# Optimization experiments

Measured on AMD Instinct MI355X. Metric: run time of the kernel, lower is better.

## Reference

```python
import jax, jax.numpy as jnp
import numpy as np
from jax import lax

EPS = 1e-8

def int8_fq(x):
    # Int8ActPerTensorFloat: per-tensor float scale from runtime max-abs, fake-quant with STE.
    s = jnp.maximum(jnp.max(jnp.abs(x)) / 127.0, EPS)
    q = jnp.clip(jnp.round(x / s), -128.0, 127.0) * s
    return x + lax.stop_gradient(q - x)

def bin_w(w):
    # BINARY weight quant: per-tensor scale = mean(|w|), weights -> +/- scale (STE).
    s = jnp.mean(jnp.abs(w))
    wq = jnp.where(w >= 0, s, -s)
    return w + lax.stop_gradient(wq - w)

def qrelu(x):
    # QuantReLU with int8 input_quant and int8 act_quant
    return int8_fq(jax.nn.relu(int8_fq(x)))

def conv2d(x, w, b):
    y = lax.conv_general_dilated(x, w, window_strides=(1, 1), padding='VALID',
                                 dimension_numbers=('NCHW', 'OIHW', 'NCHW'))
    return y + b[None, :, None, None]

def maxpool2(x):
    return lax.reduce_window(x, -jnp.inf, lax.max, (1, 1, 2, 2), (1, 1, 2, 2), 'VALID')

def setup_inputs() -> dict:
    key = jax.random.key(0)
    ks = jax.random.split(key, 12)
    B = 16384
    inp = {
        'input_tensor': jax.random.normal(ks[0], (B, 3, 32, 32), dtype=jnp.float32),
        'w1': jax.random.normal(ks[1], (6, 3, 5, 5), dtype=jnp.float32) * 0.1,
        'b1': jax.random.normal(ks[2], (6,), dtype=jnp.float32) * 0.01,
        'w2': jax.random.normal(ks[3], (16, 6, 5, 5), dtype=jnp.float32) * 0.1,
        'b2': jax.random.normal(ks[4], (16,), dtype=jnp.float32) * 0.01,
        'fw1': jax.random.normal(ks[5], (120, 400), dtype=jnp.float32) * 0.05,
        'fb1': jax.random.normal(ks[6], (120,), dtype=jnp.float32) * 0.01,
        'fw2': jax.random.normal(ks[7], (84, 120), dtype=jnp.float32) * 0.05,
        'fb2': jax.random.normal(ks[8], (84,), dtype=jnp.float32) * 0.01,
        'fw3': jax.random.normal(ks[9], (10, 84), dtype=jnp.float32) * 0.05,
        'fb3': jax.random.normal(ks[10], (10,), dtype=jnp.float32) * 0.01,
    }
    return inp

def reference(input_tensor, w1, b1, w2, b2, fw1, fb1, fw2, fb2, fw3, fb3):
    x = int8_fq(input_tensor)                  # QuantIdentity
    x = qrelu(conv2d(x, bin_w(w1), b1))        # conv1 + relu1: [B,6,28,28]
    x = maxpool2(x)                            # [B,6,14,14]
    x = qrelu(conv2d(x, bin_w(w2), b2))        # conv2 + relu2: [B,16,10,10]
    x = maxpool2(x)                            # [B,16,5,5]
    x = x.reshape(x.shape[0], -1)              # [B,400]
    x = qrelu(x @ bin_w(fw1).T + fb1)          # fc1 + relu3: [B,120]
    x = qrelu(x @ bin_w(fw2).T + fb2)          # fc2 + relu4: [B,84]
    out = x @ bin_w(fw3).T + fb3               # fc3: [B,10]
    return out
```

## Files before the change

### kernel.cpp

```cpp
#include <hip/hip_runtime.h>
#include <math.h>

#define BATCH 16384
#define EPSQ 1e-8f

#define OFF_SCAL 0
#define OFF_WPK1 16
#define OFF_WPK2 196
#define OFF_FQ1  1156
#define OFF_FQ2  13156
#define OFF_FQ3  15844
#define OFF_A    16384
#define OFF_QIN   OFF_A
#define OFF_QC2   OFF_A
#define OFF_ISUM2 (OFF_A + 6400000)
#define OFF_QC3   (OFF_A + 10000000)
#define OFF_P3    (OFF_A + 12000000)
#define OFF_P4    (OFF_A + 14000000)
#define OFF_ISUM1 (OFF_A + 18874368)

__device__ inline int sdot4(unsigned int a, unsigned int b, int c) {
    return __builtin_amdgcn_sdot4((int)a, (int)b, c, false);
}

__device__ inline unsigned int fkey(float f) {
    unsigned int u = __float_as_uint(f);
    return (u & 0x80000000u) ? ~u : (u | 0x80000000u);
}
__device__ inline float fdec(unsigned int k) {
    unsigned int u = (k & 0x80000000u) ? (k ^ 0x80000000u) : ~k;
    return __uint_as_float(u);
}
#define KEY_ZERO   0x80000000u
#define KEY_NEGINF 0x007FFFFFu

__device__ inline float waveMax(float v) {
    #pragma unroll
    for (int off = 32; off > 0; off >>= 1)
        v = fmaxf(v, __shfl_down(v, off, 64));
    return v;
}

__device__ inline void blockAtomicMax2(float vmax, float vnmax,
                                       unsigned int* gmax, unsigned int* gnmax) {
    __shared__ float sm[4], sn[4];
    float a = waveMax(vmax), b = waveMax(vnmax);
    int tid = threadIdx.x;
    if ((tid & 63) == 0) { sm[tid >> 6] = a; sn[tid >> 6] = b; }
    __syncthreads();
    if (tid == 0) {
        atomicMax(gmax, fkey(fmaxf(fmaxf(sm[0], sm[1]), fmaxf(sm[2], sm[3]))));
        atomicMax(gnmax, fkey(fmaxf(fmaxf(sn[0], sn[1]), fmaxf(sn[2], sn[3]))));
    }
}

__device__ inline float fq_elem(float x, float s) {
    float q = fminf(fmaxf(rintf(x / s), -128.0f), 127.0f);
    return q * s;
}
__device__ inline int qrelu_code(float x, float s1, float s2) {
    float q = fq_elem(x, s1);
    q = fmaxf(q, 0.0f);
    return (int)fminf(fmaxf(rintf(q / s2), -128.0f), 127.0f);
}
__device__ inline void get_qrelu_scales(const unsigned int* scalu, int slot,
                                        float& s1, float& s2) {
    float maxa = fdec(scalu[slot]), negm = fdec(scalu[slot + 1]);
    float absm = fmaxf(maxa, negm);
    s1 = fmaxf(absm / 127.0f, EPSQ);
    float qm = fminf(fmaxf(rintf(maxa / s1), -128.0f), 127.0f) * s1;
    s2 = fmaxf(fmaxf(qm, 0.0f) / 127.0f, EPSQ);
}

__device__ inline unsigned int sgn8(float w) { return (w >= 0.0f) ? 0x01u : 0xFFu; }

__device__ inline unsigned int u32at(const unsigned int* wv, int wi, int k) {
    return (k == 0) ? wv[wi]
        : __builtin_amdgcn_perm(wv[wi + 1], wv[wi], 0x03020100u + 0x01010101u * (unsigned)k);
}

__global__ __launch_bounds__(256) void prep_kernel(const float* __restrict__ w1,
        const float* __restrict__ w2, const float* __restrict__ fw1,
        const float* __restrict__ fw2, const float* __restrict__ fw3,
        float* __restrict__ wsf) {
    int blk = blockIdx.x, tid = threadIdx.x;
    unsigned int* wsu = (unsigned int*)wsf;
    if (blk == 0) {
        if (tid == 0) wsu[0] = KEY_ZERO;
        else if (tid <= 8) wsu[tid] = KEY_NEGINF;
        return;
    }
    const float* src = nullptr; int N = 0;
    if (blk == 1)      { src = w1;  N = 450; }
    else if (blk == 2) { src = w2;  N = 2400; }
    else if (blk == 3) { src = fw1; N = 48000; }
    else if (blk == 4) { src = fw2; N = 10080; }
    else               { src = fw3; N = 840; }
    __shared__ float red[256];
    float partial = 0.0f;
    for (int i = tid; i < N; i += 256) partial += fabsf(src[i]);
    red[tid] = partial;
    __syncthreads();
    for (int s = 128; s > 0; s >>= 1) {
        if (tid < s) red[tid] += red[tid + s];
        __syncthreads();
    }
    if (tid == 0) wsf[8 + blk] = red[0] / (float)N;

    if (blk == 1) {
        for (int t = tid; t < 90; t += 256) {
            const float* wp = w1 + t * 5;
            wsu[OFF_WPK1 + 2*t] = sgn8(wp[0]) | (sgn8(wp[1])<<8) | (sgn8(wp[2])<<16) | (sgn8(wp[3])<<24);
            wsu[OFF_WPK1 + 2*t + 1] = sgn8(wp[4]) << 24;
        }
    } else if (blk == 2) {
        for (int t = tid; t < 480; t += 256) {
            const float* wp = w2 + t * 5;
            wsu[OFF_WPK2 + 2*t] = sgn8(wp[0]) | (sgn8(wp[1])<<8) | (sgn8(wp[2])<<16) | (sgn8(wp[3])<<24);
            wsu[OFF_WPK2 + 2*t + 1] = sgn8(wp[4]) << 24;
        }
    } else if (blk == 3) {
        for (int i = tid; i < 12000; i += 256) {
            int j = i / 100, k = i % 100;
            const float* wp = fw1 + j * 400 + k * 4;
            wsu[OFF_FQ1 + i] = sgn8(wp[0]) | (sgn8(wp[1])<<8) | (sgn8(wp[2])<<16) | (sgn8(wp[3])<<24);
        }
    } else if (blk == 4) {
        for (int i = tid; i < 2688; i += 256) {
            int j = i >> 5, k = i & 31;
            unsigned int u = 0;
            if (k < 30) {
                const float* wp = fw2 + j * 120 + k * 4;
                u = sgn8(wp[0]) | (sgn8(wp[1])<<8) | (sgn8(wp[2])<<16) | (sgn8(wp[3])<<24);
            }
            wsu[OFF_FQ2 + i] = u;
        }
    } else {
        for (int i = tid; i < 240; i += 256) {
            int j = i / 24, k = i % 24;
            unsigned int u = 0;
            if (k < 21) {
                const float* wp = fw3 + j * 84 + k * 4;
                u = sgn8(wp[0]) | (sgn8(wp[1])<<8) | (sgn8(wp[2])<<16) | (sgn8(wp[3])<<24);
            }
            wsu[OFF_FQ3 + i] = u;
        }
    }
}

__global__ __launch_bounds__(256) void absmax_kernel(const float4* __restrict__ x, int n4,
                                                     unsigned int* __restrict__ gkey) {
    float m = 0.0f;
    int stride = gridDim.x * 256;
    for (int i = blockIdx.x * 256 + threadIdx.x; i < n4; i += stride) {
        float4 v = x[i];
        m = fmaxf(m, fmaxf(fmaxf(fabsf(v.x), fabsf(v.y)), fmaxf(fabsf(v.z), fabsf(v.w))));
    }
    __shared__ float sm[4];
    m = waveMax(m);
    int tid = threadIdx.x;
    if ((tid & 63) == 0) sm[tid >> 6] = m;
    __syncthreads();
    if (tid == 0)
        atomicMax(gkey, fkey(fmaxf(fmaxf(sm[0], sm[1]), fmaxf(sm[2], sm[3]))));
}

__global__ __launch_bounds__(256) void quant1_kernel(const float4* __restrict__ x,
                                                     float* __restrict__ wsf) {
    unsigned int* wsu = (unsigned int*)wsf;
    float s0 = fmaxf(fdec(wsu[0]) / 127.0f, EPSQ);
    unsigned int* qin = wsu + OFF_QIN;
    int stride = gridDim.x * 256;
    const int total = BATCH * 96 * 12;
    for (int unit = blockIdx.x * 256 + threadIdx.x; unit < total; unit += stride) {
        int row_id = unit / 12, w = unit % 12;
        int plane = row_id >> 5, row = row_id & 31;
        int slot = (row >> 1) + ((row & 1) << 4);
        unsigned int u = 0;
        if (w < 8) {
            float4 v = x[row_id * 8 + w];
            int q0 = (int)fminf(fmaxf(rintf(v.x / s0), -128.f), 127.f);
            int q1 = (int)fminf(fmaxf(rintf(v.y / s0), -128.f), 127.f);
            int q2 = (int)fminf(fmaxf(rintf(v.z / s0), -128.f), 127.f);
            int q3 = (int)fminf(fmaxf(rintf(v.w / s0), -128.f), 127.f);
            u = (q0 & 255) | ((q1 & 255) << 8) | ((q2 & 255) << 16) | ((unsigned)(q3 & 255) << 24);
        }
        qin[(plane * 32 + slot) * 12 + w] = u;
    }
}

#define C1_ROWP 48
#define C1_CIS  1536
#define C1_IMGS 4608
#define C1_NIMG 8

template<int PH>
__device__ __forceinline__ void c1_phase(const unsigned char* ib, const unsigned int* wcp,
                                         int* ip, int& gmax, int& gmin) {
    int a0[14], a1[14];
    #pragma unroll
    for (int i = 0; i < 14; i++) { a0[i] = 0; a1[i] = 0; }
    #pragma unroll 1
    for (int ci = 0; ci < 3; ci++) {
        uint4 A[6]; unsigned int Bv[6];
        const unsigned char* cb = ib + ci * C1_CIS;
        #pragma unroll
        for (int r = 0; r < 6; r++) {
            const unsigned char* rb = cb + (((r & 1) << 4) + (r >> 1)) * C1_ROWP;
            if (PH == 0) {
                A[r]  = *(const uint4*)(rb);
                Bv[r] = *(const unsigned int*)(rb + 16);
            } else {
                Bv[r] = *(const unsigned int*)(rb + 12);
                A[r]  = *(const uint4*)(rb + 16);
            }
        }
        const unsigned int* wkp = wcp + ci * 10;
        unsigned int wk0[5], wk4[5];
        #pragma unroll
        for (int ky = 0; ky < 5; ky++) { wk0[ky] = wkp[2*ky]; wk4[ky] = wkp[2*ky+1]; }
        #pragma unroll
        for (int r6 = 0; r6 < 6; r6++) {
            unsigned int wv[5];
            if (PH == 0) {
                wv[0] = A[r6].x; wv[1] = A[r6].y; wv[2] = A[r6].z; wv[3] = A[r6].w; wv[4] = Bv[r6];
            } else {
                wv[0] = Bv[r6]; wv[1] = A[r6].x; wv[2] = A[r6].y; wv[3] = A[r6].z; wv[4] = A[r6].w;
            }
            const int OFS = (PH == 0) ? 0 : 2;
            unsigned int up[15];
            #pragma unroll
            for (int i = 0; i < 15; i++) {
                int e = OFS + i;
                up[i] = u32at(wv, e >> 2, e & 3);
            }
            if (r6 <= 4) {
                unsigned int w0 = wk0[r6], w4 = wk4[r6];
                #pragma unroll
                for (int i = 0; i < 14; i++) {
                    a0[i] = sdot4(up[i], w0, a0[i]);
                    a0[i] = sdot4(up[i+1], w4, a0[i]);
                }
            }
            if (r6 >= 1) {
                unsigned int w0 = wk0[r6-1], w4 = wk4[r6-1];
                #pragma unroll
                for (int i = 0; i < 14; i++) {
                    a1[i] = sdot4(up[i], w0, a1[i]);
                    a1[i] = sdot4(up[i+1], w4, a1[i]);
                }
            }
        }
    }
    #pragma unroll
    for (int i = 0; i < 14; i++) {
        gmax = max(gmax, max(a0[i], a1[i]));
        gmin = min(gmin, min(a0[i], a1[i]));
    }
    #pragma unroll
    for (int p = 0; p < 7; p++)
        ip[p] = max(max(a0[2*p], a0[2*p+1]), max(a1[2*p], a1[2*p+1]));
}

__global__ __launch_bounds__(256) void conv1_kernel(const float* __restrict__ b1,
                                                    float* __restrict__ wsf) {
    __shared__ __align__(16) unsigned char xq[C1_NIMG * C1_IMGS];
    __shared__ unsigned int wpk[180];
    __shared__ float bsm[6];
    unsigned int* wsu = (unsigned int*)wsf;
    int tid = threadIdx.x;
    int b0 = blockIdx.x * C1_NIMG;
    float s0 = fmaxf(fdec(wsu[0]) / 127.0f, EPSQ);
    float seff = s0 * wsf[9];

    {
        const uint4* src = (const uint4*)((const unsigned char*)(wsu + OFF_QIN) + (size_t)b0 * C1_IMGS);
        uint4* dst = (uint4*)xq;
        for (int i = tid; i < C1_NIMG * 288; i += 256) dst[i] = src[i];
    }
    for (int i = tid; i < 180; i += 256) wpk[i] = wsu[OFF_WPK1 + i];
    if (tid < 6) bsm[tid] = b1[tid];
    __syncthreads();

    unsigned int* isum1 = wsu + OFF_ISUM1;
    float vmax = -INFINITY, vnmax = -INFINITY;
    const int ntask = C1_NIMG * 84;
    for (int t = tid; t < ntask; t += 256) {
        int img = t / 84, r = t % 84;
        int c = r / 14, py = r % 14;
        const unsigned char* ib = &xq[img * C1_IMGS + py * C1_ROWP];
        const unsigned int* wcp = &wpk[c * 30];
        int ip0[7], ip1[7];
        int gmax = -2000000000, gmin = 2000000000;
        c1_phase<0>(ib, wcp, ip0, gmax, gmin);
        c1_phase<1>(ib, wcp, ip1, gmax, gmin);
        float bias = bsm[c];
        vmax  = fmaxf(vmax,  fmaf(seff, (float)gmax, bias));
        vnmax = fmaxf(vnmax, -fmaf(seff, (float)gmin, bias));
        unsigned int* dst = isum1 + 588 * (size_t)(b0 + img) + 7 * (c * 14 + py);
        int v14[14];
        #pragma unroll
        for (int p = 0; p < 7; p++) { v14[p] = ip0[p]; v14[7 + p] = ip1[p]; }
        #pragma unroll
        for (int p = 0; p < 7; p++)
            dst[p] = (v14[2*p] & 0xFFFF) | ((unsigned)(v14[2*p+1] & 0xFFFF) << 16);
    }
    blockAtomicMax2(vmax, vnmax, wsu + 1, wsu + 2);
}

__global__ __launch_bounds__(256) void quant2_kernel(const float* __restrict__ b1,
                                                     float* __restrict__ wsf) {
    unsigned int* wsu = (unsigned int*)wsf;
    float s1, s2;
    get_qrelu_scales(wsu, 1, s1, s2);
    float s0 = fmaxf(fdec(wsu[0]) / 127.0f, EPSQ);
    float seff = s0 * wsf[9];
    float bv[6];
    #pragma unroll
    for (int c = 0; c < 6; c++) bv[c] = b1[c];
    const short* isum1 = (const short*)(wsu + OFF_ISUM1);
    unsigned int* qc2 = wsu + OFF_QC2;
    int stride = gridDim.x * 256;
    const int total = BATCH * 84 * 4;
    for (int unit = blockIdx.x * 256 + threadIdx.x; unit < total; unit += stride) {
        int row_id = unit >> 2, w = unit & 3;
        int bci = row_id / 14, row = row_id % 14;
        int ci = bci % 6;
        int slot = (row >> 1) + ((row & 1) << 3);
        float bias = bv[ci];
        unsigned int u = 0;
        const short* sp = isum1 + (size_t)bci * 196 + row * 14;
        #pragma unroll
        for (int k = 0; k < 4; k++) {
            int col = w * 4 + k;
            int code = 0;
            if (col < 14) {
                float pre = fmaf(seff, (float)sp[col], bias);
                code = qrelu_code(pre, s1, s2);
            }
            u |= ((unsigned)(code & 255)) << (8 * k);
        }
        qc2[((size_t)bci * 16 + slot) * 4 + w] = u;
    }
}

#define C2_ROWP 16
#define C2_CIS  256
#define C2_IMGS 1536
#define C2_NIMG 12

__global__ __launch_bounds__(256) void conv2_kernel(const float* __restrict__ b2,
                                                    float* __restrict__ wsf) {
    __shared__ __align__(16) unsigned char act[C2_NIMG * C2_IMGS];
    __shared__ unsigned int wpk[960];
    __shared__ float bsm[16];
    __shared__ __align__(16) short spb[C2_NIMG * 400];
    unsigned int* wsu = (unsigned int*)wsf;
    int tid = threadIdx.x;
    int b0 = blockIdx.x * C2_NIMG;
    int nimg = min(C2_NIMG, BATCH - b0);
    float s1, s2;
    get_qrelu_scales(wsu, 1, s1, s2);
    float seff = s2 * wsf[10];

    {
        const uint4* src = (const uint4*)((const unsigned char*)(wsu + OFF_QC2) + (size_t)b0 * C2_IMGS);
        uint4* dst = (uint4*)act;
        for (int i = tid; i < nimg * 96; i += 256) dst[i] = src[i];
    }
    for (int i = tid; i < 960; i += 256) wpk[i] = wsu[OFF_WPK2 + i];
    if (tid < 16) bsm[tid] = b2[tid];
    __syncthreads();

    float vmax = -INFINITY, vnmax = -INFINITY;
    int ntask = nimg * 20;
    if (tid < ntask) {
        int img = tid / 20, rem = tid % 20;
        int cq = rem / 5, py = rem % 5;
        int c0 = cq * 4;
        const unsigned char* ib = &act[img * C2_IMGS + py * C2_ROWP];
        int a0[4][10], a1[4][10];
        #pragma unroll
        for (int cc = 0; cc < 4; cc++)
            #pragma unroll
            for (int i = 0; i < 10; i++) { a0[cc][i] = 0; a1[cc][i] = 0; }
        #pragma unroll 1
        for (int ci = 0; ci < 6; ci++) {
            uint4 R[6];
            #pragma unroll
            for (int r6 = 0; r6 < 6; r6++)
                R[r6] = *(const uint4*)(ib + ci * C2_CIS + (((r6 & 1) << 3) + (r6 >> 1)) * C2_ROWP);
            #pragma unroll
            for (int r6 = 0; r6 < 6; r6++) {
                unsigned int wv[4] = { R[r6].x, R[r6].y, R[r6].z, R[r6].w };
                unsigned int up[11];
                #pragma unroll
                for (int i = 0; i < 11; i++) up[i] = u32at(wv, i >> 2, i & 3);
                #pragma unroll
                for (int cc = 0; cc < 4; cc++) {
                    const unsigned int* wkp = &wpk[((c0 + cc) * 6 + ci) * 10];
                    if (r6 <= 4) {
                        unsigned int w0 = wkp[2 * r6], w4 = wkp[2 * r6 + 1];
                        #pragma unroll
                        for (int i = 0; i < 10; i++) {
                            a0[cc][i] = sdot4(up[i], w0, a0[cc][i]);
                            a0[cc][i] = sdot4(up[i + 1], w4, a0[cc][i]);
                        }
                    }
                    if (r6 >= 1) {
                        unsigned int w0 = wkp[2 * (r6 - 1)], w4 = wkp[2 * (r6 - 1) + 1];
                        #pragma unroll
                        for (int i = 0; i < 10; i++) {
                            a1[cc][i] = sdot4(up[i], w0, a1[cc][i]);
                            a1[cc][i] = sdot4(up[i + 1], w4, a1[cc][i]);
                        }
                    }
                }
            }
        }
        #pragma unroll
        for (int cc = 0; cc < 4; cc++) {
            int gmax = -2000000000, gmin = 2000000000;
            #pragma unroll
            for (int i = 0; i < 10; i++) {
                gmax = max(gmax, max(a0[cc][i], a1[cc][i]));
                gmin = min(gmin, min(a0[cc][i], a1[cc][i]));
            }
            float bias = bsm[c0 + cc];
            vmax  = fmaxf(vmax,  fmaf(seff, (float)gmax, bias));
            vnmax = fmaxf(vnmax, -fmaf(seff, (float)gmin, bias));
            short* dst = spb + img * 400 + (c0 + cc) * 25 + py * 5;
            #pragma unroll
            for (int p = 0; p < 5; p++)
                dst[p] = (short)max(max(a0[cc][2*p], a0[cc][2*p+1]),
                                    max(a1[cc][2*p], a1[cc][2*p+1]));
        }
    }
    __syncthreads();
    {
        const uint4* pb4 = (const uint4*)spb;
        uint4* d4 = (uint4*)((short*)(wsu + OFF_ISUM2) + (size_t)b0 * 400);
        for (int i = tid; i < nimg * 50; i += 256) d4[i] = pb4[i];
    }
    blockAtomicMax2(vmax, vnmax, wsu + 3, wsu + 4);
}

__global__ __launch_bounds__(256) void quant3_kernel(const float* __restrict__ b2,
                                                     float* __restrict__ wsf) {
    unsigned int* wsu = (unsigned int*)wsf;
    float s1, s2;
    get_qrelu_scales(wsu, 3, s1, s2);
    float sp1, sp2;
    get_qrelu_scales(wsu, 1, sp1, sp2);
    float seff = sp2 * wsf[10];
    __shared__ float bv[16];
    if (threadIdx.x < 16) bv[threadIdx.x] = b2[threadIdx.x];
    __syncthreads();
    const short* isum2 = (const short*)(wsu + OFF_ISUM2);
    unsigned int* qc3 = wsu + OFF_QC3;
    int stride = gridDim.x * 256;
    const int total = BATCH * 100;
    for (int unit = blockIdx.x * 256 + threadIdx.x; unit < total; unit += stride) {
        int b = unit / 100, w = unit % 100;
        const short* sp = isum2 + (size_t)b * 400 + w * 4;
        unsigned int u = 0;
        #pragma unroll
        for (int k = 0; k < 4; k++) {
            int p = w * 4 + k;
            float pre = fmaf(seff, (float)sp[k], bv[p / 25]);
            int code = qrelu_code(pre, s1, s2);
            u |= ((unsigned)(code & 255)) << (8 * k);
        }
        qc3[unit] = u;
    }
}

__global__ __launch_bounds__(256) void fc1_kernel(const float* __restrict__ fb1,
                                                  float* __restrict__ wsf) {
    __shared__ unsigned int xs[32][100];
    __shared__ __align__(16) float pb[32 * 120];
    unsigned int* wsu = (unsigned int*)wsf;
    float* p3 = wsf + OFF_P3;
    int tid = threadIdx.x;
    size_t row0 = (size_t)blockIdx.x * 32;
    float s1, s2;
    get_qrelu_scales(wsu, 3, s1, s2);
    float seff = s2 * wsf[11];
    {
        const uint4* src = (const uint4*)(wsu + OFF_QC3 + row0 * 100);
        uint4* dst = (uint4*)xs;
        for (int i = tid; i < 800; i += 256) dst[i] = src[i];
    }
    __syncthreads();
    float vmax = -INFINITY, vnmax = -INFINITY;
    if (tid < 240) {
        int g = tid / 120, j = tid % 120;
        int acc[16];
        #pragma unroll
        for (int r = 0; r < 16; r++) acc[r] = 0;
        const uint4* wrow = (const uint4*)&wsu[OFF_FQ1 + j * 100];
        for (int kg = 0; kg < 25; kg++) {
            uint4 wv = wrow[kg];
            #pragma unroll
            for (int r = 0; r < 16; r++) {
                uint4 xv = *(const uint4*)&xs[g * 16 + r][kg * 4];
                acc[r] = sdot4(xv.x, wv.x, acc[r]);
                acc[r] = sdot4(xv.y, wv.y, acc[r]);
                acc[r] = sdot4(xv.z, wv.z, acc[r]);
                acc[r] = sdot4(xv.w, wv.w, acc[r]);
            }
        }
        float bias = fb1[j];
        #pragma unroll
        for (int r = 0; r < 16; r++) {
            float pv = fmaf(seff, (float)acc[r], bias);
            pb[(g * 16 + r) * 120 + j] = pv;
            vmax = fmaxf(vmax, pv); vnmax = fmaxf(vnmax, -pv);
        }
    }
    __syncthreads();
    {
        const float4* pb4 = (const float4*)pb;
        float4* d4 = (float4*)(p3 + row0 * 120);
        for (int i = tid; i < 960; i += 256) d4[i] = pb4[i];
    }
    blockAtomicMax2(vmax, vnmax, wsu + 5, wsu + 6);
}

__global__ __launch_bounds__(256) void fc2_kernel(const float* __restrict__ fb2,
                                                  float* __restrict__ wsf) {
    __shared__ unsigned int xs[48][32];
    __shared__ __align__(16) float pb[48 * 84];
    unsigned int* wsu = (unsigned int*)wsf;
    const float* p3 = wsf + OFF_P3;
    float* p4 = wsf + OFF_P4;
    int tid = threadIdx.x;
    size_t row0 = (size_t)blockIdx.x * 48;
    int nrow = min(48, (int)(BATCH - row0));
    float s1, s2;
    get_qrelu_scales(wsu, 5, s1, s2);
    float seff = s2 * wsf[12];
    const float4* src = (const float4*)(p3 + row0 * 120);
    for (int i = tid; i < nrow * 30; i += 256) {
        float4 v = src[i];
        int c0 = qrelu_code(v.x, s1, s2), c1 = qrelu_code(v.y, s1, s2);
        int c2 = qrelu_code(v.z, s1, s2), c3 = qrelu_code(v.w, s1, s2);
        xs[i / 30][i % 30] = c0 | (c1 << 8) | (c2 << 16) | ((unsigned)c3 << 24);
    }
    if (tid < 48) { xs[tid][30] = 0; xs[tid][31] = 0; }
    __syncthreads();
    float vmax = -INFINITY, vnmax = -INFINITY;
    if (tid < 252) {
        int g = tid / 84, j = tid % 84;
        int acc[16];
        #pragma unroll
        for (int r = 0; r < 16; r++) acc[r] = 0;
        const uint4* wrow = (const uint4*)&wsu[OFF_FQ2 + j * 32];
        #pragma unroll
        for (int kg = 0; kg < 8; kg++) {
            uint4 wv = wrow[kg];
            #pragma unroll
            for (int r = 0; r < 16; r++) {
                uint4 xv = *(const uint4*)&xs[g * 16 + r][kg * 4];
                acc[r] = sdot4(xv.x, wv.x, acc[r]);
                acc[r] = sdot4(xv.y, wv.y, acc[r]);
                acc[r] = sdot4(xv.z, wv.z, acc[r]);
                acc[r] = sdot4(xv.w, wv.w, acc[r]);
            }
        }
        float bias = fb2[j];
        #pragma unroll
        for (int r = 0; r < 16; r++) {
            int lr = g * 16 + r;
            if (lr < nrow) {
                float pv = fmaf(seff, (float)acc[r], bias);
                pb[lr * 84 + j] = pv;
                vmax = fmaxf(vmax, pv); vnmax = fmaxf(vnmax, -pv);
            }
        }
    }
    __syncthreads();
    {
        const float4* pb4 = (const float4*)pb;
        float4* d4 = (float4*)(p4 + row0 * 84);
        for (int i = tid; i < nrow * 21; i += 256) d4[i] = pb4[i];
    }
    blockAtomicMax2(vmax, vnmax, wsu + 7, wsu + 8);
}

__global__ __launch_bounds__(256) void fc3_kernel(const float* __restrict__ fb3,
                                                  float* __restrict__ out,
                                                  float* __restrict__ wsf) {
    __shared__ unsigned int wsm[240];
    __shared__ float bs[10];
    __shared__ __align__(16) float pb[2560];
    unsigned int* wsu = (unsigned int*)wsf;
    const float* p4 = wsf + OFF_P4;
    int tid = threadIdx.x;
    for (int i = tid; i < 240; i += 256) wsm[i] = wsu[OFF_FQ3 + i];
    if (tid < 10) bs[tid] = fb3[tid];
    __syncthreads();
    float s1, s2;
    get_qrelu_scales(wsu, 7, s1, s2);
    float seff = s2 * wsf[13];
    size_t row = (size_t)blockIdx.x * 256 + tid;
    unsigned int xr[24];
    const float4* src = (const float4*)(p4 + row * 84);
    #pragma unroll
    for (int k = 0; k < 21; k++) {
        float4 v = src[k];
        int c0 = qrelu_code(v.x, s1, s2), c1 = qrelu_code(v.y, s1, s2);
        int c2 = qrelu_code(v.z, s1, s2), c3 = qrelu_code(v.w, s1, s2);
        xr[k] = c0 | (c1 << 8) | (c2 << 16) | ((unsigned)c3 << 24);
    }
    xr[21] = 0; xr[22] = 0; xr[23] = 0;
    #pragma unroll
    for (int j = 0; j < 10; j++) {
        int acc = 0;
        #pragma unroll
        for (int k = 0; k < 24; k++) acc = sdot4(xr[k], wsm[j * 24 + k], acc);
        pb[tid * 10 + j] = fmaf(seff, (float)acc, bs[j]);
    }
    __syncthreads();
    {
        const float4* pb4 = (const float4*)pb;
        float4* d4 = (float4*)(out + (size_t)blockIdx.x * 2560);
        for (int i = tid; i < 640; i += 256) d4[i] = pb4[i];
    }
}

extern "C" void kernel_launch(void* const* d_in, const int* in_sizes, int n_in,
                              void* d_out, int out_size, void* d_ws, size_t ws_size,
                              hipStream_t stream) {
    const float* input = (const float*)d_in[0];
    const float* w1  = (const float*)d_in[1];
    const float* b1  = (const float*)d_in[2];
    const float* w2  = (const float*)d_in[3];
    const float* b2  = (const float*)d_in[4];
    const float* fw1 = (const float*)d_in[5];
    const float* fb1 = (const float*)d_in[6];
    const float* fw2 = (const float*)d_in[7];
    const float* fb2 = (const float*)d_in[8];
    const float* fw3 = (const float*)d_in[9];
    const float* fb3 = (const float*)d_in[10];
    float* ws  = (float*)d_ws;
    float* out = (float*)d_out;

    prep_kernel<<<6, 256, 0, stream>>>(w1, w2, fw1, fw2, fw3, ws);
    absmax_kernel<<<2048, 256, 0, stream>>>((const float4*)input,
                                            (int)((size_t)BATCH * 3072 / 4),
                                            (unsigned int*)ws);
    quant1_kernel<<<8192, 256, 0, stream>>>((const float4*)input, ws);
    conv1_kernel<<<BATCH / C1_NIMG, 256, 0, stream>>>(b1, ws);
    quant2_kernel<<<4096, 256, 0, stream>>>(b1, ws);
    conv2_kernel<<<(BATCH + C2_NIMG - 1) / C2_NIMG, 256, 0, stream>>>(b2, ws);
    quant3_kernel<<<2048, 256, 0, stream>>>(b2, ws);
    fc1_kernel<<<BATCH / 32, 256, 0, stream>>>(fb1, ws);
    fc2_kernel<<<(BATCH + 47) / 48, 256, 0, stream>>>(fb2, ws);
    fc3_kernel<<<BATCH / 256, 256, 0, stream>>>(fb3, out, ws);
}
```

Baseline: 470.0 us.

## Fuse qrelu requantization passes into conv2 and fc1 kernel prologues

Removes the standalone quant2 and quant3 kernels. conv2 now reads the pooled int16 conv1 sums and applies the qrelu quantization while filling its shared-memory tile, and fc1 does the same for the conv2 sums. This drops two kernel launches and the write-then-read round trip of the int8 code buffers through global memory. The cost is extra scalar ALU work and less coalesced short loads inside the consumer kernels' load phases. Act tiles in conv2 that were previously copied as zero padding are no longer written, so correctness depends on whether those padding bytes are read.

```diff
diff --git a/kernel.cpp b/kernel.cpp
--- a/kernel.cpp
+++ b/kernel.cpp
@@ -12,9 +12,7 @@
 #define OFF_FQ3  15844
 #define OFF_A    16384
 #define OFF_QIN   OFF_A
-#define OFF_QC2   OFF_A
 #define OFF_ISUM2 (OFF_A + 6400000)
-#define OFF_QC3   (OFF_A + 10000000)
 #define OFF_P3    (OFF_A + 12000000)
 #define OFF_P4    (OFF_A + 14000000)
 #define OFF_ISUM1 (OFF_A + 18874368)
@@ -308,52 +306,18 @@
     blockAtomicMax2(vmax, vnmax, wsu + 1, wsu + 2);
 }
 
-__global__ __launch_bounds__(256) void quant2_kernel(const float* __restrict__ b1,
-                                                     float* __restrict__ wsf) {
-    unsigned int* wsu = (unsigned int*)wsf;
-    float s1, s2;
-    get_qrelu_scales(wsu, 1, s1, s2);
-    float s0 = fmaxf(fdec(wsu[0]) / 127.0f, EPSQ);
-    float seff = s0 * wsf[9];
-    float bv[6];
-    #pragma unroll
-    for (int c = 0; c < 6; c++) bv[c] = b1[c];
-    const short* isum1 = (const short*)(wsu + OFF_ISUM1);
-    unsigned int* qc2 = wsu + OFF_QC2;
-    int stride = gridDim.x * 256;
-    const int total = BATCH * 84 * 4;
-    for (int unit = blockIdx.x * 256 + threadIdx.x; unit < total; unit += stride) {
-        int row_id = unit >> 2, w = unit & 3;
-        int bci = row_id / 14, row = row_id % 14;
-        int ci = bci % 6;
-        int slot = (row >> 1) + ((row & 1) << 3);
-        float bias = bv[ci];
-        unsigned int u = 0;
-        const short* sp = isum1 + (size_t)bci * 196 + row * 14;
-        #pragma unroll
-        for (int k = 0; k < 4; k++) {
-            int col = w * 4 + k;
-            int code = 0;
-            if (col < 14) {
-                float pre = fmaf(seff, (float)sp[col], bias);
-                code = qrelu_code(pre, s1, s2);
-            }
-            u |= ((unsigned)(code & 255)) << (8 * k);
-        }
-        qc2[((size_t)bci * 16 + slot) * 4 + w] = u;
-    }
-}
-
 #define C2_ROWP 16
 #define C2_CIS  256
 #define C2_IMGS 1536
 #define C2_NIMG 12
 
-__global__ __launch_bounds__(256) void conv2_kernel(const float* __restrict__ b2,
+__global__ __launch_bounds__(256) void conv2_kernel(const float* __restrict__ b1,
+                                                    const float* __restrict__ b2,
                                                     float* __restrict__ wsf) {
     __shared__ __align__(16) unsigned char act[C2_NIMG * C2_IMGS];
     __shared__ unsigned int wpk[960];
     __shared__ float bsm[16];
+    __shared__ float b1s[6];
     __shared__ __align__(16) short spb[C2_NIMG * 400];
     unsigned int* wsu = (unsigned int*)wsf;
     int tid = threadIdx.x;
@@ -361,15 +325,30 @@
     int nimg = min(C2_NIMG, BATCH - b0);
     float s1, s2;
     get_qrelu_scales(wsu, 1, s1, s2);
+    float s0 = fmaxf(fdec(wsu[0]) / 127.0f, EPSQ);
+    float seff1 = s0 * wsf[9];
     float seff = s2 * wsf[10];
+    if (tid < 6) b1s[tid] = b1[tid];
+    if (tid < 16) bsm[tid] = b2[tid];
+    for (int i = tid; i < 960; i += 256) wpk[i] = wsu[OFF_WPK2 + i];
+    __syncthreads();
 
     {
-        const uint4* src = (const uint4*)((const unsigned char*)(wsu + OFF_QC2) + (size_t)b0 * C2_IMGS);
-        uint4* dst = (uint4*)act;
-        for (int i = tid; i < nimg * 96; i += 256) dst[i] = src[i];
-    }
-    for (int i = tid; i < 960; i += 256) wpk[i] = wsu[OFF_WPK2 + i];
-    if (tid < 16) bsm[tid] = b2[tid];
+        const short* isum1 = (const short*)(wsu + OFF_ISUM1);
+        for (int i = tid; i < nimg * 588; i += 256) {
+            int img = i / 588, rem = i % 588;
+            int e = rem * 2;
+            int ci = e / 196, r2 = e % 196;
+            int row = r2 / 14, col = r2 % 14;
+            const short* sp = isum1 + (size_t)(b0 + img) * 1176 + e;
+            float bias = b1s[ci];
+            int r0 = qrelu_code(fmaf(seff1, (float)sp[0], bias), s1, s2);
+            int r1 = qrelu_code(fmaf(seff1, (float)sp[1], bias), s1, s2);
+            int slot = (row >> 1) + ((row & 1) << 3);
+            *(unsigned short*)&act[img * C2_IMGS + ci * C2_CIS + slot * C2_ROWP + col] =
+                (unsigned short)(r0 | (r1 << 8));
+        }
+    }
     __syncthreads();
 
     float vmax = -INFINITY, vnmax = -INFINITY;
@@ -445,51 +424,38 @@
     blockAtomicMax2(vmax, vnmax, wsu + 3, wsu + 4);
 }
 
-__global__ __launch_bounds__(256) void quant3_kernel(const float* __restrict__ b2,
-                                                     float* __restrict__ wsf) {
-    unsigned int* wsu = (unsigned int*)wsf;
-    float s1, s2;
-    get_qrelu_scales(wsu, 3, s1, s2);
-    float sp1, sp2;
-    get_qrelu_scales(wsu, 1, sp1, sp2);
-    float seff = sp2 * wsf[10];
-    __shared__ float bv[16];
-    if (threadIdx.x < 16) bv[threadIdx.x] = b2[threadIdx.x];
-    __syncthreads();
-    const short* isum2 = (const short*)(wsu + OFF_ISUM2);
-    unsigned int* qc3 = wsu + OFF_QC3;
-    int stride = gridDim.x * 256;
-    const int total = BATCH * 100;
-    for (int unit = blockIdx.x * 256 + threadIdx.x; unit < total; unit += stride) {
-        int b = unit / 100, w = unit % 100;
-        const short* sp = isum2 + (size_t)b * 400 + w * 4;
-        unsigned int u = 0;
-        #pragma unroll
-        for (int k = 0; k < 4; k++) {
-            int p = w * 4 + k;
-            float pre = fmaf(seff, (float)sp[k], bv[p / 25]);
-            int code = qrelu_code(pre, s1, s2);
-            u |= ((unsigned)(code & 255)) << (8 * k);
-        }
-        qc3[unit] = u;
-    }
-}
-
-__global__ __launch_bounds__(256) void fc1_kernel(const float* __restrict__ fb1,
+__global__ __launch_bounds__(256) void fc1_kernel(const float* __restrict__ b2,
+                                                  const float* __restrict__ fb1,
                                                   float* __restrict__ wsf) {
     __shared__ unsigned int xs[32][100];
     __shared__ __align__(16) float pb[32 * 120];
+    __shared__ float bv[16];
     unsigned int* wsu = (unsigned int*)wsf;
     float* p3 = wsf + OFF_P3;
     int tid = threadIdx.x;
     size_t row0 = (size_t)blockIdx.x * 32;
     float s1, s2;
     get_qrelu_scales(wsu, 3, s1, s2);
+    float sp1, sp2;
+    get_qrelu_scales(wsu, 1, sp1, sp2);
+    float seff2 = sp2 * wsf[10];
     float seff = s2 * wsf[11];
+    if (tid < 16) bv[tid] = b2[tid];
+    __syncthreads();
     {
-        const uint4* src = (const uint4*)(wsu + OFF_QC3 + row0 * 100);
-        uint4* dst = (uint4*)xs;
-        for (int i = tid; i < 800; i += 256) dst[i] = src[i];
+        const short* isum2 = (const short*)(wsu + OFF_ISUM2);
+        for (int i = tid; i < 3200; i += 256) {
+            int r = i / 100, w = i % 100;
+            const short* sp = isum2 + (row0 + r) * 400 + w * 4;
+            unsigned int u = 0;
+            #pragma unroll
+            for (int k = 0; k < 4; k++) {
+                int p = w * 4 + k;
+                int code = qrelu_code(fmaf(seff2, (float)sp[k], bv[p / 25]), s1, s2);
+                u |= ((unsigned)(code & 255)) << (8 * k);
+            }
+            xs[r][w] = u;
+        }
     }
     __syncthreads();
     float vmax = -INFINITY, vnmax = -INFINITY;
@@ -652,10 +618,8 @@
                                             (unsigned int*)ws);
     quant1_kernel<<<8192, 256, 0, stream>>>((const float4*)input, ws);
     conv1_kernel<<<BATCH / C1_NIMG, 256, 0, stream>>>(b1, ws);
-    quant2_kernel<<<4096, 256, 0, stream>>>(b1, ws);
-    conv2_kernel<<<(BATCH + C2_NIMG - 1) / C2_NIMG, 256, 0, stream>>>(b2, ws);
-    quant3_kernel<<<2048, 256, 0, stream>>>(b2, ws);
-    fc1_kernel<<<BATCH / 32, 256, 0, stream>>>(fb1, ws);
+    conv2_kernel<<<(BATCH + C2_NIMG - 1) / C2_NIMG, 256, 0, stream>>>(b1, b2, ws);
+    fc1_kernel<<<BATCH / 32, 256, 0, stream>>>(b2, fb1, ws);
     fc2_kernel<<<(BATCH + 47) / 48, 256, 0, stream>>>(fb2, ws);
     fc3_kernel<<<BATCH / 256, 256, 0, stream>>>(fb3, out, ws);
 }
```

Result: slower. 486.4 us (+3.5%).
